# Kernel tuning notes

Measured on AMD Instinct MI355X. Metric: run time of the kernel, lower is better.

The kernel has to match this reference:

```python
import jax, jax.numpy as jnp
import numpy as np

LAMBDA_COORD = 5.0
LAMBDA_NOOBJ = 0.5
EPS = 1e-16


def setup_inputs() -> dict:
    key = jax.random.key(0)
    k1, k2, k3 = jax.random.split(key, 3)
    B, HW, C = 64, 6400, 85  # 80x80 grid, 5 + 80 classes
    T = 50                   # objects per image
    predictions = jax.random.normal(k1, (B, HW, C), dtype=jnp.float32)
    targets_box = jax.random.uniform(k2, (B, T, 4), dtype=jnp.float32)  # cx, cy, w, h in [0,1)
    targets_cls = jax.random.randint(k3, (B, T), 0, 80)
    return {
        "predictions": predictions,
        "targets_box": targets_box,
        "targets_cls": targets_cls,
        "grid_h": 80,
        "grid_w": 80,
    }


def reference(predictions, targets_box, targets_cls, grid_h, grid_w):
    B, HW, C = predictions.shape
    T = targets_box.shape[1]
    H, W = grid_h, grid_w

    cx, cy, w, h = (targets_box[..., i] for i in range(4))  # each [B, T]
    gxf = jnp.floor(cx * W)
    gyf = jnp.floor(cy * H)
    gi = (gyf * W + gxf).astype(jnp.int32)  # [B, T] grid cell index

    # gather predictions at assigned cells -> [B, T, C]
    g = jnp.take_along_axis(predictions, gi[:, :, None], axis=1)

    # coordinate losses (per-object mean over the 2 components, as F.mse_loss does)
    txy = jnp.stack([cx * W - gxf, cy * H - gyf], axis=-1)           # [B, T, 2]
    xy_loss = jnp.mean((jax.nn.sigmoid(g[..., :2]) - txy) ** 2, -1)  # [B, T]
    twh = jnp.log(jnp.stack([w * W, h * H], axis=-1) + EPS)
    wh_loss = jnp.mean((g[..., 2:4] - twh) ** 2, -1)

    # objectness BCE with target 1: -log(sigmoid(p)) = softplus(-p)
    conf_loss = jax.nn.softplus(-g[..., 4])

    # class cross-entropy
    logp = jax.nn.log_softmax(g[..., 5:], axis=-1)
    cls_loss = -jnp.take_along_axis(logp, targets_cls[..., None], axis=-1)[..., 0]

    per_obj = LAMBDA_COORD * (xy_loss + wh_loss) + conf_loss + cls_loss
    obj_sum = jnp.sum(per_obj)

    # no-object loss: mean BCE(sigmoid(conf), 0) = softplus(p) over cells without objects
    obj_mask = jnp.zeros((B, HW), dtype=bool).at[jnp.arange(B)[:, None], gi].set(True)
    noobj = ~obj_mask
    sp = jax.nn.softplus(predictions[..., 4])  # [B, HW]
    noobj_per_img = jnp.sum(sp * noobj, -1) / jnp.maximum(jnp.sum(noobj, -1), 1)
    noobj_sum = LAMBDA_NOOBJ * jnp.sum(noobj_per_img)

    num_objects = B * T  # all targets are in-grid by construction
    return (obj_sum + noobj_sum) / num_objects
```

## Files before the change

kernel.cpp:

```cpp
#include <hip/hip_runtime.h>
#include <math.h>

constexpr int B_  = 64;
constexpr int HW_ = 6400;
constexpr int C_  = 85;
constexpr int T_  = 50;
constexpr int H_  = 80;
constexpr int W_  = 80;
constexpr float LC    = 5.0f;
constexpr float LN    = 0.5f;
constexpr float INV_N = 1.0f / (B_ * T_);

constexpr int CHUNKS_PER_IMG = 25;
constexpr int SCAN_BLOCKS    = B_ * CHUNKS_PER_IMG;
constexpr int OBJ_BLOCKS     = (B_ * T_) / 4;
constexpr int GRID_A         = SCAN_BLOCKS + OBJ_BLOCKS;
constexpr int NPART          = SCAN_BLOCKS + B_ * T_;

__device__ __forceinline__ float softplus_f(float x) {
    return fmaxf(x, 0.0f) + log1pf(expf(-fabsf(x)));
}

__device__ __forceinline__ unsigned long long dup_mask_for_image(
    const float* __restrict__ tbox, int b, int lane)
{
    int gio;
    if (lane < T_) {
        const float4 to = ((const float4*)tbox)[b * T_ + lane];
        gio = (int)(floorf(to.y * (float)H_) * (float)W_ +
                    floorf(to.x * (float)W_));
    } else {
        gio = 0x40000000 + lane;
    }
    bool dup = false;
    #pragma unroll
    for (int k = 0; k < T_ - 1; ++k) {
        int gk = __shfl(gio, k, 64);
        dup = dup || ((lane > k) && (gio == gk));
    }
    return __ballot(dup);
}

__global__ __launch_bounds__(256) void main_kernel(
    const float* __restrict__ pred, const float* __restrict__ tbox,
    const int* __restrict__ tcls, float* __restrict__ partial)
{
    int lane = threadIdx.x & 63;
    int wid  = threadIdx.x >> 6;
    __shared__ float ss[4];

    if (blockIdx.x < SCAN_BLOCKS) {
        int c   = blockIdx.x;
        int b   = c / CHUNKS_PER_IMG;
        int sub = c % CHUNKS_PER_IMG;

        unsigned long long dm = dup_mask_for_image(tbox, b, lane);
        int n_unique = T_ - __popcll(dm);
        float nn = fmaxf((float)(HW_ - n_unique), 1.0f);

        int cell = sub * 256 + (int)threadIdx.x;
        float conf = pred[((size_t)b * HW_ + cell) * C_ + 4];
        float s = softplus_f(conf);
        #pragma unroll
        for (int off = 32; off; off >>= 1) s += __shfl_xor(s, off, 64);
        if (lane == 0) ss[wid] = s;
        __syncthreads();
        if (threadIdx.x == 0)
            partial[c] = LN * (ss[0] + ss[1] + ss[2] + ss[3]) / nn;
    } else {
        int obj = (blockIdx.x - SCAN_BLOCKS) * 4 + wid;
        int b   = obj / T_;
        int myt = obj % T_;

        const float4 tb = ((const float4*)tbox)[obj];
        float gxf = floorf(tb.x * (float)W_);
        float gyf = floorf(tb.y * (float)H_);
        int gi = (int)(gyf * (float)W_ + gxf);

        unsigned long long dm = dup_mask_for_image(tbox, b, lane);
        bool canonical = !((dm >> myt) & 1ULL);
        int n_unique = T_ - __popcll(dm);
        float nn = fmaxf((float)(HW_ - n_unique), 1.0f);

        const float* g = pred + ((size_t)b * HW_ + gi) * C_;
        int cls = tcls[obj];

        int   c2 = lane + 64;
        float v1 = g[lane];
        float v2 = (c2 < C_) ? g[c2] : 0.0f;

        float m = -1e30f;
        if (lane >= 5) m = v1;
        if (c2 < C_)   m = fmaxf(m, v2);
        #pragma unroll
        for (int off = 32; off; off >>= 1) m = fmaxf(m, __shfl_xor(m, off, 64));
        float s = 0.0f;
        if (lane >= 5) s += expf(v1 - m);
        if (c2 < C_)   s += expf(v2 - m);
        #pragma unroll
        for (int off = 32; off; off >>= 1) s += __shfl_xor(s, off, 64);
        float lse = m + logf(s);

        float contrib = 0.0f;
        if (lane == 0) {
            float d = 1.0f / (1.0f + expf(-v1)) - (tb.x * (float)W_ - gxf);
            contrib = LC * 0.5f * d * d;
        } else if (lane == 1) {
            float d = 1.0f / (1.0f + expf(-v1)) - (tb.y * (float)H_ - gyf);
            contrib = LC * 0.5f * d * d;
        } else if (lane == 2) {
            float d = v1 - logf(tb.z * (float)W_ + 1e-16f);
            contrib = LC * 0.5f * d * d;
        } else if (lane == 3) {
            float d = v1 - logf(tb.w * (float)H_ + 1e-16f);
            contrib = LC * 0.5f * d * d;
        } else if (lane == 4) {
            contrib = softplus_f(-v1);
            if (canonical) contrib -= LN * softplus_f(v1) / nn;
        }
        if (lane == 5 + cls) contrib += lse - v1;
        if (c2   == 5 + cls) contrib += lse - v2;

        #pragma unroll
        for (int off = 32; off; off >>= 1) contrib += __shfl_xor(contrib, off, 64);
        if (lane == 0) partial[SCAN_BLOCKS + obj] = contrib;
    }
}

__global__ __launch_bounds__(256) void reduce_kernel(
    const float* __restrict__ partial, float* __restrict__ out)
{
    const float4* p4 = (const float4*)partial;
    float s = 0.0f;
    for (int i = threadIdx.x; i < NPART / 4; i += 256) {
        float4 v = p4[i];
        s += (v.x + v.y) + (v.z + v.w);
    }
    #pragma unroll
    for (int off = 32; off; off >>= 1) s += __shfl_xor(s, off, 64);

    __shared__ float ss[4];
    int wid = threadIdx.x >> 6;
    if ((threadIdx.x & 63) == 0) ss[wid] = s;
    __syncthreads();
    if (threadIdx.x == 0)
        out[0] = (ss[0] + ss[1] + ss[2] + ss[3]) * INV_N;
}

extern "C" void kernel_launch(void* const* d_in, const int* in_sizes, int n_in,
                              void* d_out, int out_size, void* d_ws, size_t ws_size,
                              hipStream_t stream) {
    const float* pred = (const float*)d_in[0];
    const float* tbox = (const float*)d_in[1];
    const int*   tcls = (const int*)d_in[2];
    float* out = (float*)d_out;
    float* partial = (float*)d_ws;

    main_kernel<<<GRID_A, 256, 0, stream>>>(pred, tbox, tcls, partial);
    reduce_kernel<<<1, 256, 0, stream>>>(partial, out);
}
```

Before: 20.82 us.

## Merge object-gather work into scan blocks, sharing the per-image duplicate mask

Drops the separate object blocks. Each wave now scans 64 cells of one image (100 waves per image), and the first 50 waves of each image also handle one target object. The duplicate-cell mask and the grid index are computed once per wave and reused for both tasks, which cuts the grid from 2400 to 1600 blocks and removes the redundant mask computation in object waves. Because a block's 4 waves always belong to one image, the per-block divisor stays valid. The cost is load imbalance, since waves with objects do the extra softmax work while the others sit idle.

```diff
diff --git a/kernel.cpp b/kernel.cpp
--- a/kernel.cpp
+++ b/kernel.cpp
@@ -11,22 +11,30 @@
 constexpr float LN    = 0.5f;
 constexpr float INV_N = 1.0f / (B_ * T_);
 
-constexpr int CHUNKS_PER_IMG = 25;
-constexpr int SCAN_BLOCKS    = B_ * CHUNKS_PER_IMG;
-constexpr int OBJ_BLOCKS     = (B_ * T_) / 4;
-constexpr int GRID_A         = SCAN_BLOCKS + OBJ_BLOCKS;
-constexpr int NPART          = SCAN_BLOCKS + B_ * T_;
+constexpr int GRID_A = 1600;
+constexpr int NPART  = GRID_A + B_ * T_;
 
 __device__ __forceinline__ float softplus_f(float x) {
     return fmaxf(x, 0.0f) + log1pf(expf(-fabsf(x)));
 }
 
-__device__ __forceinline__ unsigned long long dup_mask_for_image(
-    const float* __restrict__ tbox, int b, int lane)
+__global__ __launch_bounds__(256) void main_kernel(
+    const float* __restrict__ pred, const float* __restrict__ tbox,
+    const int* __restrict__ tcls, float* __restrict__ partial)
 {
+    int lane = threadIdx.x & 63;
+    int wid  = threadIdx.x >> 6;
+    int gw   = blockIdx.x * 4 + wid;
+    int bi   = gw / 100;
+    int wi   = gw % 100;
+    __shared__ float ss[4];
+
+    int cell = wi * 64 + lane;
+    float conf = pred[((size_t)bi * HW_ + cell) * C_ + 4];
+
     int gio;
     if (lane < T_) {
-        const float4 to = ((const float4*)tbox)[b * T_ + lane];
+        const float4 to = ((const float4*)tbox)[bi * T_ + lane];
         gio = (int)(floorf(to.y * (float)H_) * (float)W_ +
                     floorf(to.x * (float)W_));
     } else {
@@ -38,51 +46,25 @@
         int gk = __shfl(gio, k, 64);
         dup = dup || ((lane > k) && (gio == gk));
     }
-    return __ballot(dup);
-}
+    unsigned long long dm = __ballot(dup);
+    int n_unique = T_ - __popcll(dm);
+    float nn = fmaxf((float)(HW_ - n_unique), 1.0f);
 
-__global__ __launch_bounds__(256) void main_kernel(
-    const float* __restrict__ pred, const float* __restrict__ tbox,
-    const int* __restrict__ tcls, float* __restrict__ partial)
-{
-    int lane = threadIdx.x & 63;
-    int wid  = threadIdx.x >> 6;
-    __shared__ float ss[4];
+    float s = softplus_f(conf);
+    #pragma unroll
+    for (int off = 32; off; off >>= 1) s += __shfl_xor(s, off, 64);
+    if (lane == 0) ss[wid] = s;
 
-    if (blockIdx.x < SCAN_BLOCKS) {
-        int c   = blockIdx.x;
-        int b   = c / CHUNKS_PER_IMG;
-        int sub = c % CHUNKS_PER_IMG;
-
-        unsigned long long dm = dup_mask_for_image(tbox, b, lane);
-        int n_unique = T_ - __popcll(dm);
-        float nn = fmaxf((float)(HW_ - n_unique), 1.0f);
-
-        int cell = sub * 256 + (int)threadIdx.x;
-        float conf = pred[((size_t)b * HW_ + cell) * C_ + 4];
-        float s = softplus_f(conf);
-        #pragma unroll
-        for (int off = 32; off; off >>= 1) s += __shfl_xor(s, off, 64);
-        if (lane == 0) ss[wid] = s;
-        __syncthreads();
-        if (threadIdx.x == 0)
-            partial[c] = LN * (ss[0] + ss[1] + ss[2] + ss[3]) / nn;
-    } else {
-        int obj = (blockIdx.x - SCAN_BLOCKS) * 4 + wid;
-        int b   = obj / T_;
-        int myt = obj % T_;
+    if (wi < T_) {
+        int obj = bi * T_ + wi;
+        int gi  = __shfl(gio, wi, 64);
+        bool canonical = !((dm >> wi) & 1ULL);
 
         const float4 tb = ((const float4*)tbox)[obj];
         float gxf = floorf(tb.x * (float)W_);
         float gyf = floorf(tb.y * (float)H_);
-        int gi = (int)(gyf * (float)W_ + gxf);
 
-        unsigned long long dm = dup_mask_for_image(tbox, b, lane);
-        bool canonical = !((dm >> myt) & 1ULL);
-        int n_unique = T_ - __popcll(dm);
-        float nn = fmaxf((float)(HW_ - n_unique), 1.0f);
-
-        const float* g = pred + ((size_t)b * HW_ + gi) * C_;
+        const float* g = pred + ((size_t)bi * HW_ + gi) * C_;
         int cls = tcls[obj];
 
         int   c2 = lane + 64;
@@ -94,12 +76,12 @@
         if (c2 < C_)   m = fmaxf(m, v2);
         #pragma unroll
         for (int off = 32; off; off >>= 1) m = fmaxf(m, __shfl_xor(m, off, 64));
-        float s = 0.0f;
-        if (lane >= 5) s += expf(v1 - m);
-        if (c2 < C_)   s += expf(v2 - m);
+        float e = 0.0f;
+        if (lane >= 5) e += expf(v1 - m);
+        if (c2 < C_)   e += expf(v2 - m);
         #pragma unroll
-        for (int off = 32; off; off >>= 1) s += __shfl_xor(s, off, 64);
-        float lse = m + logf(s);
+        for (int off = 32; off; off >>= 1) e += __shfl_xor(e, off, 64);
+        float lse = m + logf(e);
 
         float contrib = 0.0f;
         if (lane == 0) {
@@ -123,8 +105,12 @@
 
         #pragma unroll
         for (int off = 32; off; off >>= 1) contrib += __shfl_xor(contrib, off, 64);
-        if (lane == 0) partial[SCAN_BLOCKS + obj] = contrib;
+        if (lane == 0) partial[GRID_A + obj] = contrib;
     }
+
+    __syncthreads();
+    if (threadIdx.x == 0)
+        partial[blockIdx.x] = LN * (ss[0] + ss[1] + ss[2] + ss[3]) / nn;
 }
 
 __global__ __launch_bounds__(256) void reduce_kernel(
@@ -156,6 +142,6 @@
     float* out = (float*)d_out;
     float* partial = (float*)d_ws;
 
-    main_kernel<<<GRID_A, 256, 0, stream>>>(pred, tbox, tcls, partial);
-    reduce_kernel<<<1, 256, 0, stream>>>(partial, out);
+    main_kernel  <<<GRID_A, 256, 0, stream>>>(pred, tbox, tcls, partial);
+    reduce_kernel<<<1,      256, 0, stream>>>(partial, out);
 }
```

Result: slower. 23.45 us (+12.6%).
